# Kernel optimization log

Measured on AMD Instinct MI355X. Metric: run time of the kernel, lower is better.

The kernel has to match this reference:

```python
import jax, jax.numpy as jnp
import numpy as np

V = 12288      # HEALPix vertices (nside=32)
C_IN = 128
C_OUT = 128
K = 4          # Chebyshev polynomial degree
DEG = 9        # nnz per Laplacian row (8 neighbors + self)
B = 8
BN_EPS = 1e-5


def setup_inputs() -> dict:
    key = jax.random.key(0)
    kx, kc, kv, kw = jax.random.split(key, 4)
    x = jax.random.normal(kx, (B, V, C_IN), dtype=jnp.float32)
    # sparse Laplacian as COO edge list: 9 entries per row
    lap_rows = jnp.repeat(jnp.arange(V, dtype=jnp.int32), DEG)          # [E]
    lap_cols = jax.random.randint(kc, (V * DEG,), 0, V, dtype=jnp.int32)
    lap_vals = jax.random.normal(kv, (V * DEG,), dtype=jnp.float32) * 0.1
    # Chebyshev weight [Fin*K, Fout] (Fin-major, K-minor, matching [B,V,Fin,K] reshape)
    weight = jax.random.normal(kw, (C_IN * K, C_OUT), dtype=jnp.float32) * (1.0 / np.sqrt(C_IN * K))
    gamma = jnp.ones((C_OUT,), dtype=jnp.float32)
    beta = jnp.zeros((C_OUT,), dtype=jnp.float32)
    return {"x": x, "lap_rows": lap_rows, "lap_cols": lap_cols,
            "lap_vals": lap_vals, "weight": weight, "gamma": gamma, "beta": beta}


def reference(x, lap_rows, lap_cols, lap_vals, weight, gamma, beta):
    b, v, c = x.shape
    k = weight.shape[0] // c

    def spmm(y):
        # y: [B, V, C] -> L @ y along vertex dim
        y2 = y.transpose(1, 0, 2).reshape(v, b * c)                 # [V, B*C]
        g = lap_vals[:, None] * y2[lap_cols]                        # [E, B*C]
        out = jnp.zeros((v, b * c), dtype=y.dtype).at[lap_rows].add(g)
        return out.reshape(v, b, c).transpose(1, 0, 2)              # [B, V, C]

    # Chebyshev recursion: T0 = x, T1 = L x, Tk = 2 L T_{k-1} - T_{k-2}
    terms = [x]
    if k > 1:
        terms.append(spmm(x))
    for _ in range(2, k):
        terms.append(2.0 * spmm(terms[-1]) - terms[-2])
    xk = jnp.stack(terms, axis=-1)                                  # [B, V, C, K]
    conv = jnp.einsum('bvck,cko->bvo', xk.reshape(b, v, c, k),
                      weight.reshape(c, k, -1))                     # [B, V, Cout]

    # BatchNorm1d over [B, Cout, V]: stats over (batch, vertices) per channel
    h = conv.transpose(0, 2, 1)                                     # [B, Cout, V]
    mean = jnp.mean(h, axis=(0, 2), keepdims=True)
    var = jnp.var(h, axis=(0, 2), keepdims=True)
    hn = (h - mean) * jax.lax.rsqrt(var + BN_EPS)
    return hn * gamma[None, :, None] + beta[None, :, None]          # [B, Cout, V]
```

## Files before the change

kernel.cpp:

```cpp
#include <hip/hip_runtime.h>

#define NV    12288
#define CIN   128
#define COUT  128
#define DEG   9
#define NB    8
#define NROWS (NB * NV)
#define KTOT  512
#define BM    384

typedef unsigned short bfu;
typedef __attribute__((ext_vector_type(8))) short short8;
typedef __attribute__((ext_vector_type(4))) float floatx4;

__device__ __forceinline__ float bf2f(unsigned short u) {
    union { unsigned int i; float f; } x;
    x.i = ((unsigned int)u) << 16;
    return x.f;
}
__device__ __forceinline__ unsigned short f2bf(float f) {
    union { float f; unsigned int i; } x;
    x.f = f;
    unsigned int r = x.i + 0x7FFFu + ((x.i >> 16) & 1u);
    return (unsigned short)(r >> 16);
}
__device__ __forceinline__ void gload16(const void* g, void* l) {
    __builtin_amdgcn_global_load_lds(
        (const __attribute__((address_space(1))) unsigned int*)g,
        (__attribute__((address_space(3))) unsigned int*)l, 16, 0, 0);
}

__global__ __launch_bounds__(256)
void prep_kernel(const float* __restrict__ x, bfu* __restrict__ xb,
                 const float* __restrict__ W, bfu* __restrict__ Wt,
                 float* __restrict__ stats)
{
    const int blk = blockIdx.x;
    const int t   = threadIdx.x;
    if (blk < 6144) {
        const size_t i = ((size_t)blk * 256 + t) * 8;
        const float4 a = *reinterpret_cast<const float4*>(x + i);
        const float4 b = *reinterpret_cast<const float4*>(x + i + 4);
        short8 r;
        r[0] = (short)f2bf(a.x); r[1] = (short)f2bf(a.y);
        r[2] = (short)f2bf(a.z); r[3] = (short)f2bf(a.w);
        r[4] = (short)f2bf(b.x); r[5] = (short)f2bf(b.y);
        r[6] = (short)f2bf(b.z); r[7] = (short)f2bf(b.w);
        *reinterpret_cast<short8*>(xb + i) = r;
    } else if (blk < 6400) {
        const int i = (blk - 6144) * 256 + t;
        const int o = i >> 9;
        const int kap = i & 511;
        const int s = kap >> 7;
        const int c = kap & 127;
        Wt[i] = f2bf(W[(size_t)(c * 4 + s) * COUT + o]);
    } else {
        stats[t] = 0.f;
        if (t == 0) stats[2 * COUT] = 0.f;
    }
}

__global__ __launch_bounds__(256)
void spmm_bf16(const bfu* __restrict__ src, const bfu* __restrict__ sub,
               bfu* __restrict__ outp, const int* __restrict__ cols,
               const float* __restrict__ vals)
{
    const int t  = threadIdx.x;
    const int b  = blockIdx.x & 7;
    const int vt = blockIdx.x >> 3;
    const int v0 = vt * 32 + (t >> 4);
    const int v1 = v0 + 16;
    const int c0 = (t & 15) * 8;

    int   ec0[DEG], ec1[DEG];
    float ev0[DEG], ev1[DEG];
#pragma unroll
    for (int e = 0; e < DEG; ++e) {
        ec0[e] = cols[v0 * DEG + e];
        ev0[e] = vals[v0 * DEG + e];
        ec1[e] = cols[v1 * DEG + e];
        ev1[e] = vals[v1 * DEG + e];
    }

    float a0[8], a1[8];
#pragma unroll
    for (int j = 0; j < 8; ++j) { a0[j] = 0.f; a1[j] = 0.f; }

    const size_t bbase = (size_t)b * NV * CIN;
#pragma unroll
    for (int e = 0; e < DEG; ++e) {
        const short8 s0 = *reinterpret_cast<const short8*>(
            src + bbase + (size_t)ec0[e] * CIN + c0);
        const short8 s1 = *reinterpret_cast<const short8*>(
            src + bbase + (size_t)ec1[e] * CIN + c0);
#pragma unroll
        for (int j = 0; j < 8; ++j) {
            a0[j] = fmaf(ev0[e], bf2f((unsigned short)s0[j]), a0[j]);
            a1[j] = fmaf(ev1[e], bf2f((unsigned short)s1[j]), a1[j]);
        }
    }

    if (sub != nullptr) {
        const short8 u0 = *reinterpret_cast<const short8*>(
            sub + bbase + (size_t)v0 * CIN + c0);
        const short8 u1 = *reinterpret_cast<const short8*>(
            sub + bbase + (size_t)v1 * CIN + c0);
#pragma unroll
        for (int j = 0; j < 8; ++j) {
            a0[j] = 2.f * a0[j] - bf2f((unsigned short)u0[j]);
            a1[j] = 2.f * a1[j] - bf2f((unsigned short)u1[j]);
        }
    }

    short8 r0, r1;
#pragma unroll
    for (int j = 0; j < 8; ++j) {
        r0[j] = (short)f2bf(a0[j]);
        r1[j] = (short)f2bf(a1[j]);
    }
    *reinterpret_cast<short8*>(outp + bbase + (size_t)v0 * CIN + c0) = r0;
    *reinterpret_cast<short8*>(outp + bbase + (size_t)v1 * CIN + c0) = r1;
}

__global__ __launch_bounds__(512, 2)
void gemm_mfma(const bfu* __restrict__ A0, const bfu* __restrict__ A1,
               const bfu* __restrict__ A2, const bfu* __restrict__ A3,
               const bfu* __restrict__ Wt, float* __restrict__ gstats,
               const float* __restrict__ gamma, const float* __restrict__ beta,
               float* __restrict__ outp)
{
    extern __shared__ char smem[];

    const int t    = threadIdx.x;
    const int lane = t & 63;
    const int wid  = t >> 6;
    const int wr   = wid >> 1;
    const int wc   = wid & 1;
    const int rbase = blockIdx.x * BM;

    floatx4 acc[6][4];
#pragma unroll
    for (int m = 0; m < 6; ++m)
#pragma unroll
        for (int n = 0; n < 4; ++n) acc[m][n] = (floatx4){0.f, 0.f, 0.f, 0.f};

    const bfu* segs[4] = {A0, A1, A2, A3};

#define STAGE(KT, BUF)                                                        \
    {                                                                         \
        const bfu* As_ = segs[(KT) >> 2];                                     \
        const int  cb_ = ((KT) & 3) * 32;                                     \
        _Pragma("unroll")                                                     \
        for (int p = 0; p < 3; ++p) {                                         \
            const int flat = p * 512 + t;                                     \
            const int rr   = flat >> 2;                                       \
            const int ck   = flat & 3;                                        \
            gload16(As_ + (size_t)(rbase + rr) * CIN + cb_                    \
                        + ((ck ^ ((rr >> 1) & 3)) << 3),                      \
                    smem + (BUF) * 24576 + flat * 16);                        \
        }                                                                     \
        {                                                                     \
            const int nn = t >> 2;                                            \
            const int ck = t & 3;                                             \
            gload16(Wt + (size_t)nn * KTOT + (KT) * 32                        \
                       + ((ck ^ ((nn >> 1) & 3)) << 3),                       \
                    smem + 73728 + (BUF) * 8192 + t * 16);                    \
        }                                                                     \
    }

    STAGE(0, 0);
    STAGE(1, 1);
    asm volatile("s_waitcnt vmcnt(4)\n\ts_barrier" ::: "memory");

    const int rsw   = ((lane & 15) >> 1) & 3;
    const int chunk = ((lane >> 4) ^ rsw) * 16;

#pragma unroll
    for (int kt = 0; kt < 16; ++kt) {
        if (kt + 2 < 16) STAGE(kt + 2, (kt + 2) % 3);

        const char* abase = smem + (kt % 3) * 24576;
        const char* bbase = smem + 73728 + (kt % 3) * 8192;
        short8 a[6], b[4];
#pragma unroll
        for (int m = 0; m < 6; ++m)
            a[m] = *reinterpret_cast<const short8*>(
                abase + (wr * 96 + m * 16 + (lane & 15)) * 64 + chunk);
#pragma unroll
        for (int n = 0; n < 4; ++n)
            b[n] = *reinterpret_cast<const short8*>(
                bbase + (wc * 64 + n * 16 + (lane & 15)) * 64 + chunk);
#pragma unroll
        for (int m = 0; m < 6; ++m)
#pragma unroll
            for (int n = 0; n < 4; ++n)
                acc[m][n] = __builtin_amdgcn_mfma_f32_16x16x32_bf16(
                    a[m], b[n], acc[m][n], 0, 0, 0);

        if (kt <= 13)
            asm volatile("s_waitcnt vmcnt(4)\n\ts_barrier" ::: "memory");
        else if (kt == 14)
            asm volatile("s_waitcnt vmcnt(0)\n\ts_barrier" ::: "memory");
    }
#undef STAGE

    __syncthreads();
    float* sred = (float*)smem;
    float* qred = sred + COUT;
    if (t < COUT) { sred[t] = 0.f; qred[t] = 0.f; }
    __syncthreads();

    const int batch = rbase / NV;
    const int v0 = (rbase % NV) + wr * 96 + (lane >> 4) * 4;
    const int ob = wc * 64 + (lane & 15);

#pragma unroll
    for (int n = 0; n < 4; ++n) {
        const int o = ob + n * 16;
        float s = 0.f, q = 0.f;
#pragma unroll
        for (int m = 0; m < 6; ++m) {
            const floatx4 v4 = acc[m][n];
#pragma unroll
            for (int j = 0; j < 4; ++j) {
                s += v4[j];
                q = fmaf(v4[j], v4[j], q);
            }
        }
        s += __shfl_xor(s, 16); s += __shfl_xor(s, 32);
        q += __shfl_xor(q, 16); q += __shfl_xor(q, 32);
        if ((lane >> 4) == 0) {
            atomicAdd(&sred[o], s);
            atomicAdd(&qred[o], q);
        }
    }
    __syncthreads();
    if (t < COUT) {
        atomicAdd(&gstats[t], sred[t]);
        atomicAdd(&gstats[COUT + t], qred[t]);
    }
    __syncthreads();

    unsigned int* ctr = (unsigned int*)&gstats[2 * COUT];
    if (t == 0) {
        __threadfence();
        atomicAdd(ctr, 1u);
        while (__hip_atomic_load(ctr, __ATOMIC_RELAXED,
                                 __HIP_MEMORY_SCOPE_AGENT) < gridDim.x) { }
        __threadfence();
    }
    __syncthreads();

    const float invN = 1.0f / (float)NROWS;
#pragma unroll
    for (int n = 0; n < 4; ++n) {
        const int o = ob + n * 16;
        const float mean = gstats[o] * invN;
        const float var  = gstats[COUT + o] * invN - mean * mean;
        const float sc   = rsqrtf(var + 1e-5f) * gamma[o];
        const float sh   = beta[o] - mean * sc;
        float* obase = outp + ((size_t)batch * COUT + o) * NV + v0;
#pragma unroll
        for (int m = 0; m < 6; ++m) {
            const floatx4 v4 = acc[m][n];
            float4 r;
            r.x = fmaf(v4[0], sc, sh);
            r.y = fmaf(v4[1], sc, sh);
            r.z = fmaf(v4[2], sc, sh);
            r.w = fmaf(v4[3], sc, sh);
            *reinterpret_cast<float4*>(obase + m * 16) = r;
        }
    }
}

extern "C" void kernel_launch(void* const* d_in, const int* in_sizes, int n_in,
                              void* d_out, int out_size, void* d_ws, size_t ws_size,
                              hipStream_t stream)
{
    (void)in_sizes; (void)n_in; (void)out_size; (void)ws_size;

    const float* x     = (const float*)d_in[0];
    const int*   cols  = (const int*)  d_in[2];
    const float* vals  = (const float*)d_in[3];
    const float* W     = (const float*)d_in[4];
    const float* gamma = (const float*)d_in[5];
    const float* beta  = (const float*)d_in[6];
    float*       out   = (float*)d_out;

    const size_t bufE = (size_t)NB * NV * CIN;

    bfu* xb    = (bfu*)d_ws;
    bfu* t1    = xb + bufE;
    bfu* t2    = t1 + bufE;
    bfu* t3    = t2 + bufE;
    bfu* Wt    = t3 + bufE;
    float* stats = (float*)(Wt + 65536);

    const dim3 blk(256);
    const int spmm_grid = (NV / 32) * NB;

    prep_kernel <<<6401, blk, 0, stream>>>(x, xb, W, Wt, stats);

    spmm_bf16 <<<spmm_grid, blk, 0, stream>>>(xb, nullptr, t1, cols, vals);
    spmm_bf16 <<<spmm_grid, blk, 0, stream>>>(t1, xb,      t2, cols, vals);
    spmm_bf16 <<<spmm_grid, blk, 0, stream>>>(t2, t1,      t3, cols, vals);

    gemm_mfma <<<NROWS / BM, dim3(512), 98304, stream>>>(
        xb, t1, t2, t3, Wt, stats, gamma, beta, out);
}
```

Measured before the change: 112.9 us.

## Fuse three SpMM launches into one persistent kernel with grid barriers

Replaces the three separate Chebyshev SpMM kernel launches with a single persistent kernel of 1024 blocks. Each block handles three vertex tiles per step, and a software grid barrier (an atomic counter stored in the stats buffer) separates the recursion steps. The goal is to remove launch gaps and tail effects between the dependent steps. In exchange it relies on all 1024 blocks being co-resident to avoid deadlock, and it adds spin-wait barrier overhead.

```diff
diff --git a/kernel.cpp b/kernel.cpp
--- a/kernel.cpp
+++ b/kernel.cpp
@@ -8,6 +8,7 @@
 #define NROWS (NB * NV)
 #define KTOT  512
 #define BM    384
+#define NBLK_SP 1024
 
 typedef unsigned short bfu;
 typedef __attribute__((ext_vector_type(8))) short short8;
@@ -56,19 +57,16 @@
         Wt[i] = f2bf(W[(size_t)(c * 4 + s) * COUT + o]);
     } else {
         stats[t] = 0.f;
-        if (t == 0) stats[2 * COUT] = 0.f;
-    }
-}
-
-__global__ __launch_bounds__(256)
-void spmm_bf16(const bfu* __restrict__ src, const bfu* __restrict__ sub,
-               bfu* __restrict__ outp, const int* __restrict__ cols,
-               const float* __restrict__ vals)
-{
-    const int t  = threadIdx.x;
-    const int b  = blockIdx.x & 7;
-    const int vt = blockIdx.x >> 3;
-    const int v0 = vt * 32 + (t >> 4);
+        if (t < 2) stats[2 * COUT + t] = 0.f;
+    }
+}
+
+__device__ __forceinline__
+void spmm_tile2(const bfu* __restrict__ src, const bfu* __restrict__ sub,
+                bfu* __restrict__ outp, const int* __restrict__ cols,
+                const float* __restrict__ vals, int b, int vtile, int t)
+{
+    const int v0 = vtile * 32 + (t >> 4);
     const int v1 = v0 + 16;
     const int c0 = (t & 15) * 8;
 
@@ -120,6 +118,45 @@
     }
     *reinterpret_cast<short8*>(outp + bbase + (size_t)v0 * CIN + c0) = r0;
     *reinterpret_cast<short8*>(outp + bbase + (size_t)v1 * CIN + c0) = r1;
+}
+
+__device__ __forceinline__ void gridbar(unsigned int* ctr, unsigned int target)
+{
+    __syncthreads();
+    if (threadIdx.x == 0) {
+        __threadfence();
+        atomicAdd(ctr, 1u);
+        while (__hip_atomic_load(ctr, __ATOMIC_RELAXED,
+                                 __HIP_MEMORY_SCOPE_AGENT) < target) { }
+        __threadfence();
+    }
+    __syncthreads();
+}
+
+__global__ __launch_bounds__(256, 4)
+void spmm3_fused(const bfu* __restrict__ xb, bfu* __restrict__ t1,
+                 bfu* __restrict__ t2, bfu* __restrict__ t3,
+                 const int* __restrict__ cols, const float* __restrict__ vals,
+                 float* __restrict__ stats)
+{
+    unsigned int* ctr = (unsigned int*)&stats[2 * COUT + 1];
+    const int t  = threadIdx.x;
+    const int b  = blockIdx.x & 7;
+    const int tg = (int)(blockIdx.x >> 3);
+
+#pragma unroll
+    for (int i = 0; i < 3; ++i)
+        spmm_tile2(xb, nullptr, t1, cols, vals, b, tg * 3 + i, t);
+    gridbar(ctr, 1 * NBLK_SP);
+
+#pragma unroll
+    for (int i = 0; i < 3; ++i)
+        spmm_tile2(t1, xb, t2, cols, vals, b, tg * 3 + i, t);
+    gridbar(ctr, 2 * NBLK_SP);
+
+#pragma unroll
+    for (int i = 0; i < 3; ++i)
+        spmm_tile2(t2, t1, t3, cols, vals, b, tg * 3 + i, t);
 }
 
 __global__ __launch_bounds__(512, 2)
@@ -297,13 +334,10 @@
     float* stats = (float*)(Wt + 65536);
 
     const dim3 blk(256);
-    const int spmm_grid = (NV / 32) * NB;
 
     prep_kernel <<<6401, blk, 0, stream>>>(x, xb, W, Wt, stats);
 
-    spmm_bf16 <<<spmm_grid, blk, 0, stream>>>(xb, nullptr, t1, cols, vals);
-    spmm_bf16 <<<spmm_grid, blk, 0, stream>>>(t1, xb,      t2, cols, vals);
-    spmm_bf16 <<<spmm_grid, blk, 0, stream>>>(t2, t1,      t3, cols, vals);
+    spmm3_fused <<<NBLK_SP, blk, 0, stream>>>(xb, t1, t2, t3, cols, vals, stats);
 
     gemm_mfma <<<NROWS / BM, dim3(512), 98304, stream>>>(
         xb, t1, t2, t3, Wt, stats, gamma, beta, out);
```

After: 416.0 us. 3.68x slower.
